# Performance work log

Hardware: AMD Instinct MI355X
Metric: run time of the kernel (lower is better)

Reference implementation:

```python
import jax, jax.numpy as jnp
import numpy as np

T = 8192   # sequence length (steps)
H = 1024   # hidden_size


def _unif(key, shape, scale):
    return jax.random.uniform(key, shape, minval=-scale, maxval=scale, dtype=jnp.float32)


def setup_inputs() -> dict:
    key = jax.random.key(0)
    ks = jax.random.split(key, 14)
    s_in = 1.0 / np.sqrt(1.0)   # nn.Linear(1, H) init bound
    s_h = 1.0 / np.sqrt(H)      # LSTM / Linear(H, 1) init bound
    d = {}
    d["inputs"] = jax.random.normal(ks[0], (T, 1), dtype=jnp.float32)
    # input projection: Linear(1, H)
    d["W_in"] = _unif(ks[1], (H, 1), s_in)
    d["b_in"] = _unif(ks[2], (H,), s_in)
    # LSTM layer 0 (gate order i, f, g, o as in PyTorch)
    d["W_ih0"] = _unif(ks[3], (4 * H, H), s_h)
    d["W_hh0"] = _unif(ks[4], (4 * H, H), s_h)
    d["b_ih0"] = _unif(ks[5], (4 * H,), s_h)
    d["b_hh0"] = _unif(ks[6], (4 * H,), s_h)
    # LSTM layer 1
    d["W_ih1"] = _unif(ks[7], (4 * H, H), s_h)
    d["W_hh1"] = _unif(ks[8], (4 * H, H), s_h)
    d["b_ih1"] = _unif(ks[9], (4 * H,), s_h)
    d["b_hh1"] = _unif(ks[10], (4 * H,), s_h)
    # output projection: Linear(H, 1)
    d["W_out"] = _unif(ks[11], (1, H), s_h)
    d["b_out"] = _unif(ks[12], (1,), s_h)
    return d


def _lstm_cell(x, h, c, W_ih, W_hh, b):
    # x, h, c: [H]; W_ih, W_hh: [4H, H]; b: [4H]
    gates = x @ W_ih.T + h @ W_hh.T + b
    i, f, g, o = jnp.split(gates, 4, axis=-1)
    c_new = jax.nn.sigmoid(f) * c + jax.nn.sigmoid(i) * jnp.tanh(g)
    h_new = jax.nn.sigmoid(o) * jnp.tanh(c_new)
    return h_new, c_new


def reference(inputs, W_in, b_in, W_ih0, W_hh0, b_ih0, b_hh0,
              W_ih1, W_hh1, b_ih1, b_hh1, W_out, b_out):
    # Teacher forcing (force=True): per-step input is inputs[i].
    # Vectorize the per-step input projection across all timesteps: [T, H]
    x_all = inputs @ W_in.T + b_in
    b0 = b_ih0 + b_hh0
    b1 = b_ih1 + b_hh1

    def step(carry, x):
        h0, c0, h1, c1 = carry
        h0, c0 = _lstm_cell(x, h0, c0, W_ih0, W_hh0, b0)
        h1, c1 = _lstm_cell(h0, h1, c1, W_ih1, W_hh1, b1)
        return (h0, c0, h1, c1), h1

    z = jnp.zeros((H,), dtype=x_all.dtype)
    (h0, c0, h1, c1), hs = jax.lax.scan(step, (z, z, z, z), x_all)
    # Vectorized output projection: [T, 1] -> [T, 1, 1] to match torch outputs
    outputs = (hs @ W_out.T + b_out)[:, None, :]
    return outputs
```

## Files before the change

### kernel.cpp

```cpp
#include <hip/hip_runtime.h>

#define T_STEPS 8192
#define HDIM 1024
#define NL0 64
#define NL1 128
#define NWG (NL0 + NL1)
#define RMASK 63
#define PVALVE 400000L
typedef unsigned long long u64;

__device__ __forceinline__ float wred(float v) {
#pragma unroll
    for (int s = 32; s >= 1; s >>= 1) v += __shfl_xor(v, s, 64);
    return v;
}
__device__ __forceinline__ int wred_min(int v) {
#pragma unroll
    for (int s = 32; s >= 1; s >>= 1) v = min(v, __shfl_xor(v, s, 64));
    return v;
}
__device__ __forceinline__ float sigm(float x) { return 1.0f / (1.0f + expf(-x)); }

__device__ __forceinline__ void st_coh_i32(int* p, int v) {
    asm volatile("global_store_dword %0, %1, off sc0 sc1" :: "v"(p), "v"(v) : "memory");
}
__device__ __forceinline__ int ld_coh_i32(const int* p) {
    int v;
    asm volatile("global_load_dword %0, %1, off sc0 sc1\n\ts_waitcnt vmcnt(0)"
                 : "=&v"(v) : "v"(p) : "memory");
    return v;
}
__device__ __forceinline__ void st_pair(u64* p, u64 v) {
    asm volatile("global_store_dwordx2 %0, %1, off sc0 sc1" :: "v"(p), "v"(v) : "memory");
}
__device__ __forceinline__ u64 ld_p8(const u64* p) {
    u64 v;
    asm volatile("global_load_dwordx2 %0, %1, off sc0 sc1\n\ts_waitcnt vmcnt(0)"
                 : "=&v"(v) : "v"(p) : "memory");
    return v;
}
__device__ __forceinline__ void ld2p2(const u64* p0, const u64* p1, u64& a, u64& b) {
    asm volatile(
        "global_load_dwordx2 %0, %2, off sc0 sc1\n\t"
        "global_load_dwordx2 %1, %3, off sc0 sc1\n\t"
        "s_waitcnt vmcnt(0)"
        : "=&v"(a), "=&v"(b) : "v"(p0), "v"(p1) : "memory");
}
__device__ __forceinline__ void ld3i(const int* p, int& a, int& b, int& c) {
    asm volatile(
        "global_load_dword %0, %3, off sc0 sc1\n\t"
        "global_load_dword %1, %3, off offset:256 sc0 sc1\n\t"
        "global_load_dword %2, %3, off offset:512 sc0 sc1\n\t"
        "s_waitcnt vmcnt(0)"
        : "=&v"(a), "=&v"(b), "=&v"(c) : "v"(p) : "memory");
}
__device__ __forceinline__ u64 pack(float h, int tag) {
    return ((u64)(unsigned)tag << 32) | (u64)__float_as_uint(h);
}
__device__ __forceinline__ float pval(u64 q) { return __uint_as_float((unsigned)q); }
__device__ __forceinline__ unsigned ptag(u64 q) { return (unsigned)(q >> 32); }

__global__ void lstm_prologue(const float* __restrict__ Wih0, const float* __restrict__ Win,
                              const float* __restrict__ bin, const float* __restrict__ bih0,
                              const float* __restrict__ bhh0, const float* __restrict__ bih1,
                              const float* __restrict__ bhh1,
                              float* __restrict__ U, float* __restrict__ V, float* __restrict__ B1) {
    const int wv = threadIdx.x >> 6, lane = threadIdx.x & 63;
    const int r = blockIdx.x * 4 + wv;
    const float* wp = Wih0 + (size_t)r * HDIM;
    float au = 0.f, av = 0.f;
#pragma unroll
    for (int j = 0; j < 16; ++j) {
        float wj = wp[lane + 64 * j];
        au += wj * Win[lane + 64 * j];
        av += wj * bin[lane + 64 * j];
    }
    au = wred(au);
    av = wred(av);
    if (lane == 0) {
        U[r] = au;
        V[r] = av + bih0[r] + bhh0[r];
        B1[r] = bih1[r] + bhh1[r];
    }
}

__global__ __launch_bounds__(1024, 1) void lstm_persistent(
    const float* __restrict__ inputs, const float* __restrict__ Whh0,
    const float* __restrict__ Wih1, const float* __restrict__ Whh1,
    const float* __restrict__ Wout, int* flags, u64* h0q, u64* h1q,
    const float* __restrict__ U, const float* __restrict__ V, const float* __restrict__ B1,
    float* part) {
    __shared__ float kb0[2][1024];
    __shared__ float kb1[2][1024];
    __shared__ float ibuf[T_STEPS];
    __shared__ float psum[16][4];
    __shared__ float bld[32], wolds[8];
    __shared__ float osum[2];
    __shared__ int lds_ab;
    const int tid = threadIdx.x;
    const int wv = tid >> 6;
    const int lane = tid & 63;
    const int wg = blockIdx.x;
    int* abp = flags + 1024;
    const int* frep = flags + 256 + (wg & 31) * 16;

    if (wg == NWG) {
        if (tid >= 64) return;
        long it = 0;
        for (;;) {
            int a, b, c;
            ld3i(flags + lane, a, b, c);
            int m = wred_min(min(a, min(b, c)));
            if (lane < 32) st_coh_i32(flags + 256 + lane * 16, m);
            if (m >= T_STEPS) break;
            asm volatile("s_sleep 1");
            if ((++it & 63) == 0) {
                if (ld_coh_i32(abp)) break;
                if (it > PVALVE) { if (lane == 0) st_coh_i32(abp, 1); break; }
            }
        }
        return;
    }

    if (tid == 0) lds_ab = 0;

    if (wg < NL0) {
        const int e0 = wg * 16 + wv;
        float w0[4][16], uu[4], vv[4];
#pragma unroll
        for (int g = 0; g < 4; ++g) {
            const int row = g * HDIM + e0;
            const float* pw = Whh0 + (size_t)row * HDIM;
#pragma unroll
            for (int k = 0; k < 16; ++k) w0[g][k] = pw[lane + 64 * k];
            uu[g] = U[row];
            vv[g] = V[row];
        }
#pragma unroll
        for (int k = 0; k < 8; ++k) ibuf[tid + 1024 * k] = inputs[tid + 1024 * k];
        __syncthreads();

        float c0 = 0.f;
        for (int p = 0; p < T_STEPS; ++p) {
            const int par = p & 1;
            u64 q = 0;
            if (p > 0) {
                const u64* src = h0q + (size_t)((p - 1) & RMASK) * 1024 + tid;
                const unsigned xt = (unsigned)p;
                bool need = true;
                long it = 0;
                for (;;) {
                    if (!__ballot(need)) break;
                    if (need) { q = ld_p8(src); need = (ptag(q) != xt); }
                    if ((++it & 255) == 0) {
                        if (ld_coh_i32(abp) || it > PVALVE) {
                            st_coh_i32(abp, 1); lds_ab = 1; break;
                        }
                    }
                }
            }
            kb0[par][tid] = pval(q);
            __syncthreads();
            if (lds_ab) break;
            if ((p & 3) == 3 && tid == 0) st_coh_i32(flags + wg, p + 1);
            float hv[16];
#pragma unroll
            for (int j = 0; j < 16; ++j) hv[j] = kb0[par][lane + 64 * j];
            float acc[4];
#pragma unroll
            for (int g = 0; g < 4; ++g) {
                float s = 0.f;
#pragma unroll
                for (int k = 0; k < 16; ++k) s += w0[g][k] * hv[k];
                acc[g] = s;
            }
#pragma unroll
            for (int g = 0; g < 4; ++g) acc[g] = wred(acc[g]);
            const float st = ibuf[p];
            const float gi = acc[0] + st * uu[0] + vv[0];
            const float gf = acc[1] + st * uu[1] + vv[1];
            const float gg = acc[2] + st * uu[2] + vv[2];
            const float go = acc[3] + st * uu[3] + vv[3];
            const float cn = sigm(gf) * c0 + sigm(gi) * tanhf(gg);
            const float hn = sigm(go) * tanhf(cn);
            c0 = cn;
            if (p >= 48 && (p & 7) == 0 && lane == 0) {
                long itf = 0;
                for (;;) {
                    if (ld_coh_i32(frep) >= p - 40) break;
                    asm volatile("s_sleep 2");
                    if (ld_coh_i32(abp)) break;
                    if (++itf > PVALVE) { st_coh_i32(abp, 1); break; }
                }
            }
            if (lane == 0)
                st_pair(h0q + (size_t)(p & RMASK) * 1024 + e0, pack(hn, p + 1));
        }
        __syncthreads();
        if (tid == 0) st_coh_i32(flags + wg, T_STEPS);
    } else {
        const int wgb = wg - NL0;
        const int half = wv >> 3;
        const int ew = wv & 7;
        const int e = wgb * 8 + ew;
        const float* wsrc = half ? Whh1 : Wih1;
        float w1[4][16];
#pragma unroll
        for (int g = 0; g < 4; ++g) {
            const int row = g * HDIM + e;
            const float* pw = wsrc + (size_t)row * HDIM;
#pragma unroll
            for (int k = 0; k < 16; ++k) w1[g][k] = pw[lane + 64 * k];
        }
        if (tid < 32) bld[tid] = B1[(tid & 3) * HDIM + wgb * 8 + (tid >> 2)];
        if (tid < 8) wolds[tid] = Wout[wgb * 8 + tid];
        __syncthreads();

        float cst = 0.f;
        for (int t = 0; t < T_STEPS; ++t) {
            const int par = t & 1;
            u64 q0 = 0, q1 = 0;
            {
                const u64* s0 = h0q + (size_t)(t & RMASK) * 1024 + tid;
                const u64* s1 = h1q + (size_t)((t - 1) & RMASK) * 1024 + tid;
                const unsigned xt0 = (unsigned)(t + 1), xt1 = (unsigned)t;
                bool n0 = true, n1 = (t > 0);
                long it = 0;
                for (;;) {
                    if (!__ballot(n0 || n1)) break;
                    if (n0 || n1) {
                        u64 a, b;
                        ld2p2(s0, s1, a, b);
                        if (n0 && ptag(a) == xt0) { q0 = a; n0 = false; }
                        if (n1 && ptag(b) == xt1) { q1 = b; n1 = false; }
                    }
                    if ((++it & 255) == 0) {
                        if (ld_coh_i32(abp) || it > PVALVE) {
                            st_coh_i32(abp, 1); lds_ab = 1; break;
                        }
                    }
                }
            }
            kb0[par][tid] = pval(q0);
            kb1[par][tid] = pval(q1);
            __syncthreads();
            if (lds_ab) break;
            if (tid == 0) {
                if (t >= 1) part[(size_t)(t - 1) * 128 + wgb] = osum[(t - 1) & 1];
                if ((t & 3) == 3) st_coh_i32(flags + NL0 + wgb, t + 1);
            }
            if (t >= 48 && (t & 7) == 0 && tid == 960) {
                long itf = 0;
                for (;;) {
                    if (ld_coh_i32(frep) >= t - 40) break;
                    asm volatile("s_sleep 2");
                    if (ld_coh_i32(abp)) break;
                    if (++itf > PVALVE) { st_coh_i32(abp, 1); break; }
                }
            }
            float hv[16];
            const float* kb = half ? kb1[par] : kb0[par];
#pragma unroll
            for (int j = 0; j < 16; ++j) hv[j] = kb[lane + 64 * j];
            float acc[4];
#pragma unroll
            for (int g = 0; g < 4; ++g) {
                float s = 0.f;
#pragma unroll
                for (int k = 0; k < 16; ++k) s += w1[g][k] * hv[k];
                acc[g] = s;
            }
#pragma unroll
            for (int g = 0; g < 4; ++g) acc[g] = wred(acc[g]);
            if (lane == 0) {
                psum[wv][0] = acc[0]; psum[wv][1] = acc[1];
                psum[wv][2] = acc[2]; psum[wv][3] = acc[3];
            }
            __syncthreads();
            if (wv == 0) {
                float wos = 0.f;
                if (lane < 8) {
                    const float gi = psum[lane][0] + psum[lane + 8][0] + bld[lane * 4 + 0];
                    const float gf = psum[lane][1] + psum[lane + 8][1] + bld[lane * 4 + 1];
                    const float gg = psum[lane][2] + psum[lane + 8][2] + bld[lane * 4 + 2];
                    const float go = psum[lane][3] + psum[lane + 8][3] + bld[lane * 4 + 3];
                    const float cn = sigm(gf) * cst + sigm(gi) * tanhf(gg);
                    const float hn = sigm(go) * tanhf(cn);
                    cst = cn;
                    st_pair(h1q + (size_t)(t & RMASK) * 1024 + wgb * 8 + lane, pack(hn, t + 1));
                    wos = wolds[lane] * hn;
                }
                wos += __shfl_xor(wos, 1, 64);
                wos += __shfl_xor(wos, 2, 64);
                wos += __shfl_xor(wos, 4, 64);
                if (lane == 0) osum[t & 1] = wos;
            }
        }
        __syncthreads();
        if (tid == 0) {
            part[(size_t)(T_STEPS - 1) * 128 + wgb] = osum[(T_STEPS - 1) & 1];
            st_coh_i32(flags + NL0 + wgb, T_STEPS);
        }
    }
}

__global__ void lstm_finalize(const float* __restrict__ part, const float* __restrict__ bout,
                              float* __restrict__ out) {
    const int t = blockIdx.x * 256 + threadIdx.x;
    if (t < T_STEPS) {
        const float4* p4 = (const float4*)(part + (size_t)t * 128);
        float s = bout[0];
#pragma unroll
        for (int i = 0; i < 32; ++i) {
            float4 v = p4[i];
            s += v.x + v.y + v.z + v.w;
        }
        out[t] = s;
    }
}

extern "C" void kernel_launch(void* const* d_in, const int* in_sizes, int n_in,
                              void* d_out, int out_size, void* d_ws, size_t ws_size,
                              hipStream_t stream) {
    const float* inputs = (const float*)d_in[0];
    const float* Win  = (const float*)d_in[1];
    const float* bin  = (const float*)d_in[2];
    const float* Wih0 = (const float*)d_in[3];
    const float* Whh0 = (const float*)d_in[4];
    const float* bih0 = (const float*)d_in[5];
    const float* bhh0 = (const float*)d_in[6];
    const float* Wih1 = (const float*)d_in[7];
    const float* Whh1 = (const float*)d_in[8];
    const float* bih1 = (const float*)d_in[9];
    const float* bhh1 = (const float*)d_in[10];
    const float* Wout = (const float*)d_in[11];
    const float* bout = (const float*)d_in[12];

    char* ws = (char*)d_ws;
    int*  flags = (int*)ws;
    u64*  h0q   = (u64*)(ws + 8192);
    u64*  h1q   = (u64*)(ws + 8192 + 524288);
    float* U    = (float*)(ws + 1056768);
    float* V    = (float*)(ws + 1073152);
    float* B1   = (float*)(ws + 1089536);
    float* part = (float*)(ws + 1105920);

    if (ws_size < (size_t)5300224) return;

    hipMemsetAsync(ws, 0, 8192, stream);

    lstm_prologue<<<1024, 256, 0, stream>>>(Wih0, Win, bin, bih0, bhh0, bih1, bhh1, U, V, B1);
    lstm_persistent<<<NWG + 1, 1024, 0, stream>>>(inputs, Whh0, Wih1, Whh1, Wout,
                                                  flags, h0q, h1q, U, V, B1, part);
    lstm_finalize<<<(T_STEPS + 255) / 256, 256, 0, stream>>>(part, bout, (float*)d_out);
}
```

Baseline: 38.64 ms.

## Replace per-thread tag polling with aggregated atomic counters and single-wave publishing

Each persistent workgroup used to have all 1024 threads spin on tagged hidden-state values in global memory. Now one wave polls a small set of per-slot arrival counters and releases the other waves through an LDS flag, after which they read the now-ready data. Producers gather their outputs in LDS and publish them from a single wave, which then does an atomic counter increment. The goal is less coherent global polling traffic and latency on the per-step critical path, at the cost of an extra intra-workgroup handoff and an atomic per step.

```diff
diff --git a/kernel.cpp b/kernel.cpp
--- a/kernel.cpp
+++ b/kernel.cpp
@@ -5,7 +5,6 @@
 #define NL0 64
 #define NL1 128
 #define NWG (NL0 + NL1)
-#define RMASK 63
 #define PVALVE 400000L
 typedef unsigned long long u64;
 
@@ -45,6 +44,9 @@
         "global_load_dwordx2 %1, %3, off sc0 sc1\n\t"
         "s_waitcnt vmcnt(0)"
         : "=&v"(a), "=&v"(b) : "v"(p0), "v"(p1) : "memory");
+}
+__device__ __forceinline__ void at_add(int* p, int v) {
+    asm volatile("global_atomic_add %0, %1, off" :: "v"(p), "v"(v) : "memory");
 }
 __device__ __forceinline__ void ld3i(const int* p, int& a, int& b, int& c) {
     asm volatile(
@@ -87,16 +89,16 @@
 __global__ __launch_bounds__(1024, 1) void lstm_persistent(
     const float* __restrict__ inputs, const float* __restrict__ Whh0,
     const float* __restrict__ Wih1, const float* __restrict__ Whh1,
-    const float* __restrict__ Wout, int* flags, u64* h0q, u64* h1q,
+    const float* __restrict__ Wout, int* flags, int* cnt0, int* cnt1, u64* h0q, u64* h1q,
     const float* __restrict__ U, const float* __restrict__ V, const float* __restrict__ B1,
     float* part) {
-    __shared__ float kb0[2][1024];
-    __shared__ float kb1[2][1024];
+    __shared__ float kb[2][2048];
     __shared__ float ibuf[T_STEPS];
     __shared__ float psum[16][4];
+    __shared__ float hpub[16];
     __shared__ float bld[32], wolds[8];
     __shared__ float osum[2];
-    __shared__ int lds_ab;
+    __shared__ int rdy[2], pubcnt[2], lds_ab;
     const int tid = threadIdx.x;
     const int wv = tid >> 6;
     const int lane = tid & 63;
@@ -122,7 +124,7 @@
         return;
     }
 
-    if (tid == 0) lds_ab = 0;
+    if (tid == 0) { rdy[0] = -1; rdy[1] = -1; pubcnt[0] = 0; pubcnt[1] = 0; lds_ab = 0; }
 
     if (wg < NL0) {
         const int e0 = wg * 16 + wv;
@@ -143,29 +145,53 @@
         float c0 = 0.f;
         for (int p = 0; p < T_STEPS; ++p) {
             const int par = p & 1;
-            u64 q = 0;
             if (p > 0) {
-                const u64* src = h0q + (size_t)((p - 1) & RMASK) * 1024 + tid;
-                const unsigned xt = (unsigned)p;
-                bool need = true;
-                long it = 0;
-                for (;;) {
-                    if (!__ballot(need)) break;
-                    if (need) { q = ld_p8(src); need = (ptag(q) != xt); }
-                    if ((++it & 255) == 0) {
-                        if (ld_coh_i32(abp) || it > PVALVE) {
+                const int slot = (p - 1) & 63;
+                if (wv == 0) {
+                    const int tgt = 2 * (((p - 1) >> 6) + 1);
+                    const int* cp = cnt0 + slot * 128 + lane * 4;
+                    bool need = (lane < 32);
+                    long it = 0;
+                    for (;;) {
+                        if (need) need = (ld_coh_i32(cp) < tgt);
+                        if (!__ballot(need)) break;
+                        if ((++it & 63) == 0) {
+                            if (ld_coh_i32(abp) || it > PVALVE) {
+                                st_coh_i32(abp, 1); lds_ab = 1; break;
+                            }
+                        }
+                    }
+                    if (lane == 0)
+                        __hip_atomic_store(&rdy[par], p, __ATOMIC_RELEASE,
+                                           __HIP_MEMORY_SCOPE_WORKGROUP);
+                } else {
+                    long it = 0;
+                    while (__hip_atomic_load(&rdy[par], __ATOMIC_ACQUIRE,
+                                             __HIP_MEMORY_SCOPE_WORKGROUP) < p) {
+                        if (++it > 50000000L) { lds_ab = 1; break; }
+                    }
+                }
+                const u64* src = h0q + (size_t)slot * 1024 + wv * 64 + lane;
+                u64 q = ld_p8(src);
+                long it2 = 0;
+                while (ptag(q) != (unsigned)p) {
+                    q = ld_p8(src);
+                    if ((++it2 & 255) == 0) {
+                        if (ld_coh_i32(abp) || it2 > PVALVE) {
                             st_coh_i32(abp, 1); lds_ab = 1; break;
                         }
                     }
                 }
-            }
-            kb0[par][tid] = pval(q);
+                kb[par][wv * 64 + lane] = pval(q);
+            } else {
+                kb[par][wv * 64 + lane] = 0.f;
+            }
             __syncthreads();
             if (lds_ab) break;
             if ((p & 3) == 3 && tid == 0) st_coh_i32(flags + wg, p + 1);
             float hv[16];
 #pragma unroll
-            for (int j = 0; j < 16; ++j) hv[j] = kb0[par][lane + 64 * j];
+            for (int j = 0; j < 16; ++j) hv[j] = kb[par][lane + 64 * j];
             float acc[4];
 #pragma unroll
             for (int g = 0; g < 4; ++g) {
@@ -184,17 +210,33 @@
             const float cn = sigm(gf) * c0 + sigm(gi) * tanhf(gg);
             const float hn = sigm(go) * tanhf(cn);
             c0 = cn;
-            if (p >= 48 && (p & 7) == 0 && lane == 0) {
-                long itf = 0;
-                for (;;) {
-                    if (ld_coh_i32(frep) >= p - 40) break;
-                    asm volatile("s_sleep 2");
-                    if (ld_coh_i32(abp)) break;
-                    if (++itf > PVALVE) { st_coh_i32(abp, 1); break; }
-                }
-            }
-            if (lane == 0)
-                st_pair(h0q + (size_t)(p & RMASK) * 1024 + e0, pack(hn, p + 1));
+            if (lane == 0) {
+                hpub[wv] = hn;
+                __hip_atomic_fetch_add(&pubcnt[par], 1, __ATOMIC_RELEASE,
+                                       __HIP_MEMORY_SCOPE_WORKGROUP);
+            }
+            if (wv == 15) {
+                const int tgt16 = 16 * ((p >> 1) + 1);
+                long it3 = 0;
+                while (__hip_atomic_load(&pubcnt[par], __ATOMIC_ACQUIRE,
+                                         __HIP_MEMORY_SCOPE_WORKGROUP) < tgt16) {
+                    if (++it3 > 50000000L) { lds_ab = 1; break; }
+                }
+                if (p >= 48 && (p & 7) == 0 && lane < 16) {
+                    long itf = 0;
+                    for (;;) {
+                        if (ld_coh_i32(frep) >= p - 40) break;
+                        asm volatile("s_sleep 2");
+                        if (ld_coh_i32(abp)) break;
+                        if (++itf > PVALVE) { st_coh_i32(abp, 1); break; }
+                    }
+                }
+                if (lane < 16)
+                    st_pair(h0q + (size_t)(p & 63) * 1024 + wg * 16 + lane,
+                            pack(hpub[lane], p + 1));
+                asm volatile("s_waitcnt vmcnt(0)" ::: "memory");
+                if (lane == 0) at_add(cnt0 + (p & 63) * 128 + (wg >> 1) * 4, 1);
+            }
         }
         __syncthreads();
         if (tid == 0) st_coh_i32(flags + wg, T_STEPS);
@@ -219,49 +261,82 @@
         float cst = 0.f;
         for (int t = 0; t < T_STEPS; ++t) {
             const int par = t & 1;
-            u64 q0 = 0, q1 = 0;
-            {
-                const u64* s0 = h0q + (size_t)(t & RMASK) * 1024 + tid;
-                const u64* s1 = h1q + (size_t)((t - 1) & RMASK) * 1024 + tid;
-                const unsigned xt0 = (unsigned)(t + 1), xt1 = (unsigned)t;
-                bool n0 = true, n1 = (t > 0);
+            const int sl0 = t & 63, sl1 = (t - 1) & 63;
+            if (wv == 0) {
+                const int tg0 = 2 * ((t >> 6) + 1);
+                const int tg1 = 4 * (((t - 1) >> 6) + 1);
+                const int* cp = (lane < 32) ? (cnt0 + sl0 * 128 + lane * 4)
+                                            : (cnt1 + sl1 * 128 + (lane - 32) * 4);
+                const int tg = (lane < 32) ? tg0 : tg1;
+                bool need = (lane < 32) || (t > 0);
                 long it = 0;
                 for (;;) {
-                    if (!__ballot(n0 || n1)) break;
-                    if (n0 || n1) {
-                        u64 a, b;
-                        ld2p2(s0, s1, a, b);
-                        if (n0 && ptag(a) == xt0) { q0 = a; n0 = false; }
-                        if (n1 && ptag(b) == xt1) { q1 = b; n1 = false; }
-                    }
-                    if ((++it & 255) == 0) {
+                    if (need) need = (ld_coh_i32(cp) < tg);
+                    if (!__ballot(need)) break;
+                    if ((++it & 63) == 0) {
                         if (ld_coh_i32(abp) || it > PVALVE) {
                             st_coh_i32(abp, 1); lds_ab = 1; break;
                         }
                     }
                 }
-            }
-            kb0[par][tid] = pval(q0);
-            kb1[par][tid] = pval(q1);
+                if (lane == 0)
+                    __hip_atomic_store(&rdy[par], t + 1, __ATOMIC_RELEASE,
+                                       __HIP_MEMORY_SCOPE_WORKGROUP);
+            } else {
+                long it = 0;
+                while (__hip_atomic_load(&rdy[par], __ATOMIC_ACQUIRE,
+                                         __HIP_MEMORY_SCOPE_WORKGROUP) < t + 1) {
+                    if (++it > 50000000L) { lds_ab = 1; break; }
+                }
+            }
+            {
+                const int ci = (wv & 7) * 128 + lane;
+                if (!half) {
+                    const u64* s0 = h0q + (size_t)sl0 * 1024 + ci;
+                    u64 a, b;
+                    ld2p2(s0, s0 + 64, a, b);
+                    const unsigned xt = (unsigned)(t + 1);
+                    long it2 = 0;
+                    while ((ptag(a) ^ xt) | (ptag(b) ^ xt)) {
+                        ld2p2(s0, s0 + 64, a, b);
+                        if ((++it2 & 255) == 0) {
+                            if (ld_coh_i32(abp) || it2 > PVALVE) {
+                                st_coh_i32(abp, 1); lds_ab = 1; break;
+                            }
+                        }
+                    }
+                    kb[par][ci] = pval(a);
+                    kb[par][ci + 64] = pval(b);
+                } else if (t > 0) {
+                    const u64* s1 = h1q + (size_t)sl1 * 1024 + ci;
+                    u64 a, b;
+                    ld2p2(s1, s1 + 64, a, b);
+                    const unsigned xt = (unsigned)t;
+                    long it2 = 0;
+                    while ((ptag(a) ^ xt) | (ptag(b) ^ xt)) {
+                        ld2p2(s1, s1 + 64, a, b);
+                        if ((++it2 & 255) == 0) {
+                            if (ld_coh_i32(abp) || it2 > PVALVE) {
+                                st_coh_i32(abp, 1); lds_ab = 1; break;
+                            }
+                        }
+                    }
+                    kb[par][1024 + ci] = pval(a);
+                    kb[par][1024 + ci + 64] = pval(b);
+                } else {
+                    kb[par][1024 + ci] = 0.f;
+                    kb[par][1024 + ci + 64] = 0.f;
+                }
+            }
             __syncthreads();
             if (lds_ab) break;
             if (tid == 0) {
                 if (t >= 1) part[(size_t)(t - 1) * 128 + wgb] = osum[(t - 1) & 1];
                 if ((t & 3) == 3) st_coh_i32(flags + NL0 + wgb, t + 1);
             }
-            if (t >= 48 && (t & 7) == 0 && tid == 960) {
-                long itf = 0;
-                for (;;) {
-                    if (ld_coh_i32(frep) >= t - 40) break;
-                    asm volatile("s_sleep 2");
-                    if (ld_coh_i32(abp)) break;
-                    if (++itf > PVALVE) { st_coh_i32(abp, 1); break; }
-                }
-            }
             float hv[16];
-            const float* kb = half ? kb1[par] : kb0[par];
-#pragma unroll
-            for (int j = 0; j < 16; ++j) hv[j] = kb[lane + 64 * j];
+#pragma unroll
+            for (int j = 0; j < 16; ++j) hv[j] = kb[par][half * 1024 + lane + 64 * j];
             float acc[4];
 #pragma unroll
             for (int g = 0; g < 4; ++g) {
@@ -277,19 +352,32 @@
                 psum[wv][2] = acc[2]; psum[wv][3] = acc[3];
             }
             __syncthreads();
-            if (wv == 0) {
-                float wos = 0.f;
+            if (wv == 15) {
+                float hn = 0.f, wos = 0.f;
                 if (lane < 8) {
                     const float gi = psum[lane][0] + psum[lane + 8][0] + bld[lane * 4 + 0];
                     const float gf = psum[lane][1] + psum[lane + 8][1] + bld[lane * 4 + 1];
                     const float gg = psum[lane][2] + psum[lane + 8][2] + bld[lane * 4 + 2];
                     const float go = psum[lane][3] + psum[lane + 8][3] + bld[lane * 4 + 3];
                     const float cn = sigm(gf) * cst + sigm(gi) * tanhf(gg);
-                    const float hn = sigm(go) * tanhf(cn);
+                    hn = sigm(go) * tanhf(cn);
                     cst = cn;
-                    st_pair(h1q + (size_t)(t & RMASK) * 1024 + wgb * 8 + lane, pack(hn, t + 1));
+                }
+                if (t >= 48 && (t & 7) == 0 && lane < 8) {
+                    long itf = 0;
+                    for (;;) {
+                        if (ld_coh_i32(frep) >= t - 40) break;
+                        asm volatile("s_sleep 2");
+                        if (ld_coh_i32(abp)) break;
+                        if (++itf > PVALVE) { st_coh_i32(abp, 1); break; }
+                    }
+                }
+                if (lane < 8) {
+                    st_pair(h1q + (size_t)sl0 * 1024 + wgb * 8 + lane, pack(hn, t + 1));
                     wos = wolds[lane] * hn;
                 }
+                asm volatile("s_waitcnt vmcnt(0)" ::: "memory");
+                if (lane == 0) at_add(cnt1 + sl0 * 128 + (wgb >> 2) * 4, 1);
                 wos += __shfl_xor(wos, 1, 64);
                 wos += __shfl_xor(wos, 2, 64);
                 wos += __shfl_xor(wos, 4, 64);
@@ -338,19 +426,21 @@
 
     char* ws = (char*)d_ws;
     int*  flags = (int*)ws;
-    u64*  h0q   = (u64*)(ws + 8192);
-    u64*  h1q   = (u64*)(ws + 8192 + 524288);
-    float* U    = (float*)(ws + 1056768);
-    float* V    = (float*)(ws + 1073152);
-    float* B1   = (float*)(ws + 1089536);
-    float* part = (float*)(ws + 1105920);
-
-    if (ws_size < (size_t)5300224) return;
-
-    hipMemsetAsync(ws, 0, 8192, stream);
+    int*  cnt0  = (int*)(ws + 8192);
+    int*  cnt1  = (int*)(ws + 40960);
+    u64*  h0q   = (u64*)(ws + 73728);
+    u64*  h1q   = (u64*)(ws + 598016);
+    float* U    = (float*)(ws + 1122304);
+    float* V    = (float*)(ws + 1138688);
+    float* B1   = (float*)(ws + 1155072);
+    float* part = (float*)(ws + 1171456);
+
+    if (ws_size < (size_t)5365760) return;
+
+    hipMemsetAsync(ws, 0, 73728, stream);
 
     lstm_prologue<<<1024, 256, 0, stream>>>(Wih0, Win, bin, bih0, bhh0, bih1, bhh1, U, V, B1);
     lstm_persistent<<<NWG + 1, 1024, 0, stream>>>(inputs, Whh0, Wih1, Whh1, Wout,
-                                                  flags, h0q, h1q, U, V, B1, part);
+                                                  flags, cnt0, cnt1, h0q, h1q, U, V, B1, part);
     lstm_finalize<<<(T_STEPS + 255) / 256, 256, 0, stream>>>(part, bout, (float*)d_out);
 }
```

Result: slower. 48.27 ms (+24.9%).
